# Kernel optimization log

Measured on AMD Instinct MI355X. Metric: run time of the kernel, lower is better.

## Reference

```python
import math
import jax, jax.numpy as jnp
import numpy as np

D_MODEL = 1024
N_HEADS = 16
HEAD_DIM = D_MODEL // N_HEADS
ROPE_BASE = 10000.0
EPS = 1e-6


def rmsnorm(x, w, eps=EPS):
    # x: (..., head_dim); computed in fp32 like the torch code
    xf = x.astype(jnp.float32)
    rms = jax.lax.rsqrt(jnp.mean(xf * xf, axis=-1, keepdims=True) + eps)
    return (xf * rms).astype(x.dtype) * w


def apply_rope(x, cos, sin):
    # x: (B, H, T, head_dim); cos/sin: (T, head_dim/2)
    d2 = x.shape[-1] // 2
    x1, x2 = x[..., :d2], x[..., d2:]
    c = cos[None, None, :, :]
    s = sin[None, None, :, :]
    return jnp.concatenate([x1 * c - x2 * s, x2 * c + x1 * s], axis=-1)


def setup_inputs() -> dict:
    key = jax.random.key(0)
    ks = jax.random.split(key, 7)
    B, T = 2, 2048
    x = jax.random.normal(ks[0], (B, T, D_MODEL), dtype=jnp.float32)
    scale = 1.0 / math.sqrt(D_MODEL)
    Wq = jax.random.normal(ks[1], (D_MODEL, D_MODEL), dtype=jnp.float32) * scale
    Wk = jax.random.normal(ks[2], (D_MODEL, D_MODEL), dtype=jnp.float32) * scale
    Wv = jax.random.normal(ks[3], (D_MODEL, D_MODEL), dtype=jnp.float32) * scale
    Wo = jax.random.normal(ks[4], (D_MODEL, D_MODEL), dtype=jnp.float32) * scale
    q_norm_w = jnp.ones((HEAD_DIM,), dtype=jnp.float32)
    k_norm_w = jnp.ones((HEAD_DIM,), dtype=jnp.float32)
    return {"x": x, "Wq": Wq, "Wk": Wk, "Wv": Wv, "Wo": Wo,
            "q_norm_w": q_norm_w, "k_norm_w": k_norm_w}


def reference(x, Wq, Wk, Wv, Wo, q_norm_w, k_norm_w):
    B, T, d = x.shape
    H, hd = N_HEADS, HEAD_DIM
    # projections (nn.Linear applies x @ W.T; here W is stored as (in,out))
    q = (x @ Wq).reshape(B, T, H, hd).transpose(0, 2, 1, 3)  # (B,H,T,hd)
    k = (x @ Wk).reshape(B, T, H, hd).transpose(0, 2, 1, 3)
    v = (x @ Wv).reshape(B, T, H, hd).transpose(0, 2, 1, 3)
    # QK RMSNorm per head
    q = rmsnorm(q, q_norm_w)
    k = rmsnorm(k, k_norm_w)
    # rotary embeddings
    inv_freq = 1.0 / (ROPE_BASE ** (jnp.arange(0, hd, 2, dtype=jnp.float32) / hd))
    t = jnp.arange(T, dtype=jnp.float32)
    freqs = jnp.outer(t, inv_freq)  # (T, hd/2)
    cos, sin = jnp.cos(freqs), jnp.sin(freqs)
    q = apply_rope(q, cos, sin)
    k = apply_rope(k, cos, sin)
    # naive full attention with causal mask
    scale = 1.0 / math.sqrt(hd)
    attn = jnp.einsum('bhqd,bhkd->bhqk', q, k) * scale  # (B,H,T,T)
    causal = jnp.triu(jnp.full((T, T), -jnp.inf, dtype=attn.dtype), k=1)
    attn = attn + causal[None, None, :, :]
    attn = jax.nn.softmax(attn, axis=-1)
    out = jnp.einsum('bhqk,bhkd->bhqd', attn, v)
    out = out.transpose(0, 2, 1, 3).reshape(B, T, d)
    return out @ Wo
```

## Files before the change

kernel.cpp:

```cpp
#include <hip/hip_runtime.h>

typedef unsigned short u16;
typedef unsigned int   u32;
typedef __bf16 bf16x8 __attribute__((ext_vector_type(8)));
typedef float  f32x4  __attribute__((ext_vector_type(4)));
typedef u32    u32x4  __attribute__((ext_vector_type(4)));
typedef u16    u16x4  __attribute__((ext_vector_type(4)));

#define D_MODEL 1024
#define T_SEQ   2048
#define NH      16
#define HD      64

__device__ __forceinline__ float b2f(u16 u){ return __uint_as_float(((u32)u)<<16); }
__device__ __forceinline__ u16 f2b(float f){
  u32 x = __float_as_uint(f);
  x += 0x7fffu + ((x>>16)&1u);
  return (u16)(x>>16);
}

__device__ __forceinline__ void gll16(const void* g, void* l){
  __builtin_amdgcn_global_load_lds((const __attribute__((address_space(1))) unsigned int*)g,
                                   (__attribute__((address_space(3))) unsigned int*)l, 16, 0, 0);
}

__global__ __launch_bounds__(256) void f32_to_bf16(const float* __restrict__ src, u16* __restrict__ dst)
{
  const int i = (blockIdx.x*256 + threadIdx.x)<<2;
  f32x4 v = *(const f32x4*)(src + i);
  u16x4 o;
  o[0]=f2b(v[0]); o[1]=f2b(v[1]); o[2]=f2b(v[2]); o[3]=f2b(v[3]);
  *(u16x4*)(dst + i) = o;
}

__global__ void transpose_w(const float* __restrict__ W0, const float* __restrict__ W1,
                            const float* __restrict__ W2, const float* __restrict__ W3,
                            u16* __restrict__ T0, u16* __restrict__ T1,
                            u16* __restrict__ T2, u16* __restrict__ T3)
{
  __shared__ u16 s[32][33];
  const int z = blockIdx.z;
  const float* src = (z==0)?W0:(z==1)?W1:(z==2)?W2:W3;
  u16*         dst = (z==0)?T0:(z==1)?T1:(z==2)?T2:T3;
  const int x = threadIdx.x, y = threadIdx.y;
  const int r0 = blockIdx.y*32, c0 = blockIdx.x*32;
  #pragma unroll
  for (int r=0;r<4;r++) s[y + r*8][x] = f2b(src[(r0 + y + r*8)*D_MODEL + c0 + x]);
  __syncthreads();
  #pragma unroll
  for (int r=0;r<4;r++) dst[(c0 + y + r*8)*D_MODEL + r0 + x] = s[x][y + r*8];
}

__global__ __launch_bounds__(256) void gemm128(
    const u16* __restrict__ A,
    const u16* __restrict__ B0, const u16* __restrict__ B1, const u16* __restrict__ B2,
    float* __restrict__ oF, u16* __restrict__ oQ, u16* __restrict__ oK, u16* __restrict__ oVt)
{
  __shared__ __align__(16) u16 sA[512*8];
  __shared__ __align__(16) u16 sB[512*8];
  const int z = blockIdx.z;
  const u16* Bt = (z==0)?B0:(z==1)?B1:B2;

  const int tid = threadIdx.x;
  const int bm0 = blockIdx.y<<7, bn0 = blockIdx.x<<7;
  const int lane = tid & 63;
  const int w  = tid>>6;
  const int wm = (w>>1)<<6;
  const int wn = (w&1)<<6;
  const int quad = lane>>4, lr = lane&15;

  const int s0 = w*64 + lane, s1 = 256 + w*64 + lane;
  const int rA0 = s0>>2, cA0 = (s0&3)^((rA0>>1)&3);
  const int rA1 = s1>>2, cA1 = (s1&3)^((rA1>>1)&3);
  u16* ldsA0 = sA + (w*64)*8;
  u16* ldsA1 = sA + (256 + w*64)*8;
  u16* ldsB0 = sB + (w*64)*8;
  u16* ldsB1 = sB + (256 + w*64)*8;
  const u16* gA0 = A  + (bm0+rA0)*D_MODEL + cA0*8;
  const u16* gA1 = A  + (bm0+rA1)*D_MODEL + cA1*8;
  const u16* gB0 = Bt + (bn0+rA0)*D_MODEL + cA0*8;
  const u16* gB1 = Bt + (bn0+rA1)*D_MODEL + cA1*8;

  const int cfr = (lr>>1)&3;

  const f32x4 z4 = {0.f,0.f,0.f,0.f};
  f32x4 acc[4][4];
  #pragma unroll
  for (int i=0;i<4;i++)
    #pragma unroll
    for (int j=0;j<4;j++) acc[i][j] = z4;

  for (int kt=0; kt<D_MODEL; kt+=32){
    gll16(gA0 + kt, ldsA0);
    gll16(gA1 + kt, ldsA1);
    gll16(gB0 + kt, ldsB0);
    gll16(gB1 + kt, ldsB1);
    __syncthreads();
    bf16x8 af[4], bfr[4];
    const int cq = (quad ^ cfr)<<3;
    #pragma unroll
    for (int i=0;i<4;i++) af[i]  = *(const bf16x8*)(sA + (wm + (i<<4) + lr)*32 + cq);
    #pragma unroll
    for (int j=0;j<4;j++) bfr[j] = *(const bf16x8*)(sB + (wn + (j<<4) + lr)*32 + cq);
    #pragma unroll
    for (int i=0;i<4;i++)
      #pragma unroll
      for (int j=0;j<4;j++)
        acc[i][j] = __builtin_amdgcn_mfma_f32_16x16x32_bf16(af[i], bfr[j], acc[i][j], 0, 0, 0);
    __syncthreads();
  }

  const int rq = quad<<2;
  if (z==2){
    #pragma unroll
    for (int i=0;i<4;i++){
      int row0 = bm0 + wm + (i<<4) + rq;
      int bb = row0 >> 11, tt = row0 & (T_SEQ-1);
      #pragma unroll
      for (int j=0;j<4;j++){
        int col = bn0 + wn + (j<<4) + lr;
        int hh = col >> 6, dd = col & 63;
        u16x4 st;
        #pragma unroll
        for (int r=0;r<4;r++) st[r] = f2b(acc[i][j][r]);
        *(u16x4*)(oVt + ((bb*NH + hh)*HD + dd)*T_SEQ + tt) = st;
      }
    }
  } else {
    u16* oB = (z==0) ? oQ : oK;
    #pragma unroll
    for (int i=0;i<4;i++){
      #pragma unroll
      for (int r=0;r<4;r++){
        int grow = bm0 + wm + (i<<4) + rq + r;
        #pragma unroll
        for (int j=0;j<4;j++){
          int gcol = bn0 + wn + (j<<4) + lr;
          float v = acc[i][j][r];
          if (z==0 && oF) oF[grow*D_MODEL + gcol] = v;
          else            oB[grow*D_MODEL + gcol] = f2b(v);
        }
      }
    }
  }
}

__global__ __launch_bounds__(256) void rmsrope(u16* __restrict__ Q, u16* __restrict__ K,
                                               const float* __restrict__ qw, const float* __restrict__ kw)
{
  const int gtid = blockIdx.x*256 + threadIdx.x;
  const int wave = gtid >> 6;
  const int lane = gtid & 63;
  const int row  = wave >> 4;
  const int h    = wave & 15;
  const int t    = row & (T_SEQ-1);
  const int addr = row*D_MODEL + h*HD + lane;

  const int fi = lane & 31;
  const float inv_freq = __expf(-(float)fi * 0.28782313662f);
  float sn, cs;
  __sincosf((float)t * inv_freq, &sn, &cs);

  {
    float x = b2f(Q[addr]);
    float ss = x*x;
    #pragma unroll
    for (int off=32; off>=1; off>>=1) ss += __shfl_xor(ss, off, 64);
    float rms = rsqrtf(ss*(1.0f/64.0f) + 1e-6f);
    float xn = x*rms*qw[lane];
    float pr = __shfl_xor(xn, 32, 64);
    float ro = (lane<32) ? (xn*cs - pr*sn) : (xn*cs + pr*sn);
    Q[addr] = f2b(ro * 0.125f);
  }
  {
    float x = b2f(K[addr]);
    float ss = x*x;
    #pragma unroll
    for (int off=32; off>=1; off>>=1) ss += __shfl_xor(ss, off, 64);
    float rms = rsqrtf(ss*(1.0f/64.0f) + 1e-6f);
    float xn = x*rms*kw[lane];
    float pr = __shfl_xor(xn, 32, 64);
    K[addr] = f2b((lane<32) ? (xn*cs - pr*sn) : (xn*cs + pr*sn));
  }
}

__global__ __launch_bounds__(256) void attn_mfma(const u16* __restrict__ Qb, const u16* __restrict__ Kb,
                                                 const u16* __restrict__ Vt, u16* __restrict__ AO)
{
  __shared__ __align__(16) u16 sK [2][512*8];
  __shared__ __align__(16) u16 sVT[2][512*8];
  __shared__ __align__(16) u16 sP [4][16*68];
  const int tid = threadIdx.x;
  const int h  = blockIdx.x, b = blockIdx.y;
  const int qt = 31 - blockIdx.z;
  const int w = tid>>6, lane = tid&63;
  const int quad = lane>>4, lr = lane&15;
  const int q8 = quad<<3;

  const int s0 = w*64 + lane, s1 = 256 + w*64 + lane;
  const int r0s = s0>>3, c0s = (s0&7)^(r0s&7);
  const int r1s = s1>>3, c1s = (s1&7)^(r1s&7);
  const u16* Kbase = Kb + (b*T_SEQ)*D_MODEL + h*HD;
  const u16* Vbase = Vt + (b*NH + h)*HD*T_SEQ;
  const int ldsOff0 = (w*64)*8, ldsOff1 = (256 + w*64)*8;

  const u16* Qrow = Qb + (b*T_SEQ + qt*64 + w*16 + lr)*D_MODEL + h*HD;
  bf16x8 qf0 = *(const bf16x8*)(Qrow + q8);
  bf16x8 qf1 = *(const bf16x8*)(Qrow + 32 + q8);

  f32x4 o[4];
  float lp[4];
  const f32x4 z4 = {0.f,0.f,0.f,0.f};
  const f32x4 i8 = {-8.f,-8.f,-8.f,-8.f};
  #pragma unroll
  for (int r=0;r<4;r++) lp[r] = 0.f;
  #pragma unroll
  for (int nt=0;nt<4;nt++) o[nt] = z4;

  u16* myP = sP[w];

  {
    gll16(Kbase + (0*64 + r0s)*D_MODEL + c0s*8, &sK[0][ldsOff0]);
    gll16(Kbase + (0*64 + r1s)*D_MODEL + c1s*8, &sK[0][ldsOff1]);
    gll16(Vbase + r0s*T_SEQ + 0*64 + c0s*8,     &sVT[0][ldsOff0]);
    gll16(Vbase + r1s*T_SEQ + 0*64 + c1s*8,     &sVT[0][ldsOff1]);
  }
  __syncthreads();

  for (int kt=0; kt<=qt; ++kt){
    const int cur = kt&1;
    if (kt < qt){
      const int kn = kt+1, nb = cur^1;
      gll16(Kbase + (kn*64 + r0s)*D_MODEL + c0s*8, &sK[nb][ldsOff0]);
      gll16(Kbase + (kn*64 + r1s)*D_MODEL + c1s*8, &sK[nb][ldsOff1]);
      gll16(Vbase + r0s*T_SEQ + kn*64 + c0s*8,     &sVT[nb][ldsOff0]);
      gll16(Vbase + r1s*T_SEQ + kn*64 + c1s*8,     &sVT[nb][ldsOff1]);
    }

    f32x4 s4[4];
    #pragma unroll
    for (int ct=0; ct<4; ++ct){
      const int row = ct*16 + lr;
      const int sw = row&7;
      bf16x8 k0 = *(const bf16x8*)(&sK[cur][(row*8 + (quad     ^ sw))*8]);
      bf16x8 k1 = *(const bf16x8*)(&sK[cur][(row*8 + ((4+quad) ^ sw))*8]);
      f32x4 acc = i8;
      acc = __builtin_amdgcn_mfma_f32_16x16x32_bf16(qf0, k0, acc, 0,0,0);
      acc = __builtin_amdgcn_mfma_f32_16x16x32_bf16(qf1, k1, acc, 0,0,0);
      s4[ct] = acc;
    }

    if (kt == qt){
      #pragma unroll
      for (int ct=0; ct<4; ++ct){
        int col = ct*16 + lr;
        #pragma unroll
        for (int r=0;r<4;r++)
          if (col > w*16 + quad*4 + r) s4[ct][r] = -1e30f;
      }
    }

    #pragma unroll
    for (int ct=0; ct<4; ++ct){
      #pragma unroll
      for (int r=0;r<4;r++){
        float p = __expf(s4[ct][r]);
        u32 pu = __float_as_uint(p) & 0xffff0000u;
        lp[r] += __uint_as_float(pu);
        myP[(quad*4 + r)*68 + ct*16 + lr] = (u16)(pu>>16);
      }
    }

    #pragma unroll
    for (int st=0; st<2; ++st){
      bf16x8 pf = *(const bf16x8*)(myP + lr*68 + st*32 + q8);
      #pragma unroll
      for (int nt=0;nt<4;nt++){
        const int row = nt*16 + lr;
        const int slot = row*8 + ((st*4+quad) ^ (row&7));
        bf16x8 vf = *(const bf16x8*)(&sVT[cur][slot*8]);
        o[nt] = __builtin_amdgcn_mfma_f32_16x16x32_bf16(pf, vf, o[nt], 0,0,0);
      }
    }
    __syncthreads();
  }

  #pragma unroll
  for (int r=0;r<4;r++){
    #pragma unroll
    for (int off=8; off>=1; off>>=1) lp[r] += __shfl_xor(lp[r], off, 64);
  }
  const int rowg = b*T_SEQ + qt*64 + w*16 + quad*4;
  #pragma unroll
  for (int r=0;r<4;r++){
    float inv = 1.0f / lp[r];
    #pragma unroll
    for (int nt=0;nt<4;nt++)
      AO[(rowg + r)*D_MODEL + h*HD + nt*16 + lr] = f2b(o[nt][r]*inv);
  }
}

extern "C" void kernel_launch(void* const* d_in, const int* in_sizes, int n_in,
                              void* d_out, int out_size, void* d_ws, size_t ws_size,
                              hipStream_t stream)
{
  const float* X  = (const float*)d_in[0];
  const float* Wq = (const float*)d_in[1];
  const float* Wk = (const float*)d_in[2];
  const float* Wv = (const float*)d_in[3];
  const float* Wo = (const float*)d_in[4];
  const float* qw = (const float*)d_in[5];
  const float* kw = (const float*)d_in[6];

  char* ws = (char*)d_ws;
  const size_t MB = 1024*1024;
  u16* WqT = (u16*)(ws + 0*MB);
  u16* WkT = (u16*)(ws + 2*MB);
  u16* WvT = (u16*)(ws + 4*MB);
  u16* WoT = (u16*)(ws + 6*MB);
  u16* Xb  = (u16*)(ws + 8*MB);
  u16* Qb  = (u16*)(ws + 16*MB);
  u16* Kb  = (u16*)(ws + 24*MB);
  u16* Vt  = (u16*)(ws + 32*MB);
  u16* AO  = (u16*)(ws + 40*MB);

  f32_to_bf16<<<dim3(4096), 256, 0, stream>>>(X, Xb);
  transpose_w<<<dim3(32,32,4), dim3(32,8), 0, stream>>>(Wq,Wk,Wv,Wo, WqT,WkT,WvT,WoT);
  gemm128<<<dim3(8,32,3), 256, 0, stream>>>(Xb, WqT, WkT, WvT, nullptr, Qb, Kb, Vt);
  rmsrope<<<dim3(16384), 256, 0, stream>>>(Qb, Kb, qw, kw);
  attn_mfma<<<dim3(NH, 2, 32), 256, 0, stream>>>(Qb, Kb, Vt, AO);
  gemm128<<<dim3(8,32,1), 256, 0, stream>>>(AO, WoT, WoT, WoT, (float*)d_out, nullptr, nullptr, nullptr);
}
```

Measured before the change: 230.2 us.

## Fuse RMSNorm and RoPE into QKV GEMM epilogue with XCD-aware tiling

Removes the separate rmsrope pass by applying per-head RMSNorm and rotary embedding inside the QKV GEMM epilogue, using a precomputed cos/sin table written by a small new kernel. The QKV weights are packed contiguously so a single GEMM covers all three projections. Both GEMMs now use a 64-wide K step with 8-way LDS swizzle and a block-id remap that groups tiles by XCD for better L2 locality. This saves one read-modify-write pass over Q and K and halves the number of barriers, at the cost of more LDS per block and a heavier epilogue.

```diff
diff --git a/kernel.cpp b/kernel.cpp
--- a/kernel.cpp
+++ b/kernel.cpp
@@ -4,6 +4,7 @@
 typedef unsigned int   u32;
 typedef __bf16 bf16x8 __attribute__((ext_vector_type(8)));
 typedef float  f32x4  __attribute__((ext_vector_type(4)));
+typedef float  f32x2  __attribute__((ext_vector_type(2)));
 typedef u32    u32x4  __attribute__((ext_vector_type(4)));
 typedef u16    u16x4  __attribute__((ext_vector_type(4)));
 
@@ -51,37 +52,46 @@
   for (int r=0;r<4;r++) dst[(c0 + y + r*8)*D_MODEL + r0 + x] = s[x][y + r*8];
 }
 
-__global__ __launch_bounds__(256) void gemm128(
-    const u16* __restrict__ A,
-    const u16* __restrict__ B0, const u16* __restrict__ B1, const u16* __restrict__ B2,
-    float* __restrict__ oF, u16* __restrict__ oQ, u16* __restrict__ oK, u16* __restrict__ oVt)
-{
-  __shared__ __align__(16) u16 sA[512*8];
-  __shared__ __align__(16) u16 sB[512*8];
-  const int z = blockIdx.z;
-  const u16* Bt = (z==0)?B0:(z==1)?B1:B2;
+__global__ __launch_bounds__(256) void rope_table(float* __restrict__ cs)
+{
+  const int gid = blockIdx.x*256 + threadIdx.x;
+  const int t = gid >> 5, fi = gid & 31;
+  const float invf = expf(-(float)fi * 0.2878231366242558f);
+  float sn, cn;
+  sincosf((float)t * invf, &sn, &cn);
+  cs[gid*2]   = cn;
+  cs[gid*2+1] = sn;
+}
+
+__global__ __launch_bounds__(256) void gemm_qkv(
+    const u16* __restrict__ A, const u16* __restrict__ Bt,
+    const float* __restrict__ qw, const float* __restrict__ kw,
+    const float* __restrict__ cs,
+    u16* __restrict__ Qb, u16* __restrict__ Kb, u16* __restrict__ Vt)
+{
+  __shared__ __align__(16) u16 sA[1024*8];
+  __shared__ __align__(16) u16 sB[1024*8];
+  const int id = blockIdx.x;
+  const int xcd = id & 7, slot = id >> 3;
+  const int bn = (xcd & 1)*12 + (slot % 12);
+  const int bm = (xcd >> 1)*8 + (slot / 12);
+  const int bm0 = bm<<7, bn0 = bn<<7;
 
   const int tid = threadIdx.x;
-  const int bm0 = blockIdx.y<<7, bn0 = blockIdx.x<<7;
   const int lane = tid & 63;
   const int w  = tid>>6;
   const int wm = (w>>1)<<6;
   const int wn = (w&1)<<6;
   const int quad = lane>>4, lr = lane&15;
-
-  const int s0 = w*64 + lane, s1 = 256 + w*64 + lane;
-  const int rA0 = s0>>2, cA0 = (s0&3)^((rA0>>1)&3);
-  const int rA1 = s1>>2, cA1 = (s1&3)^((rA1>>1)&3);
-  u16* ldsA0 = sA + (w*64)*8;
-  u16* ldsA1 = sA + (256 + w*64)*8;
-  u16* ldsB0 = sB + (w*64)*8;
-  u16* ldsB1 = sB + (256 + w*64)*8;
-  const u16* gA0 = A  + (bm0+rA0)*D_MODEL + cA0*8;
-  const u16* gA1 = A  + (bm0+rA1)*D_MODEL + cA1*8;
-  const u16* gB0 = Bt + (bn0+rA0)*D_MODEL + cA0*8;
-  const u16* gB1 = Bt + (bn0+rA1)*D_MODEL + cA1*8;
-
-  const int cfr = (lr>>1)&3;
+  const int swl = lr & 7;
+
+  int rS[4], cS[4];
+  #pragma unroll
+  for (int i=0;i<4;i++){
+    int s = i*256 + tid;
+    rS[i] = s>>3;
+    cS[i] = (s&7) ^ (rS[i]&7);
+  }
 
   const f32x4 z4 = {0.f,0.f,0.f,0.f};
   f32x4 acc[4][4];
@@ -90,97 +100,157 @@
     #pragma unroll
     for (int j=0;j<4;j++) acc[i][j] = z4;
 
-  for (int kt=0; kt<D_MODEL; kt+=32){
-    gll16(gA0 + kt, ldsA0);
-    gll16(gA1 + kt, ldsA1);
-    gll16(gB0 + kt, ldsB0);
-    gll16(gB1 + kt, ldsB1);
+  for (int kt=0; kt<D_MODEL; kt+=64){
+    #pragma unroll
+    for (int i=0;i<4;i++)
+      gll16(A  + (bm0+rS[i])*D_MODEL + kt + cS[i]*8, sA + (i*256 + w*64)*8);
+    #pragma unroll
+    for (int i=0;i<4;i++)
+      gll16(Bt + (bn0+rS[i])*D_MODEL + kt + cS[i]*8, sB + (i*256 + w*64)*8);
     __syncthreads();
-    bf16x8 af[4], bfr[4];
-    const int cq = (quad ^ cfr)<<3;
-    #pragma unroll
-    for (int i=0;i<4;i++) af[i]  = *(const bf16x8*)(sA + (wm + (i<<4) + lr)*32 + cq);
-    #pragma unroll
-    for (int j=0;j<4;j++) bfr[j] = *(const bf16x8*)(sB + (wn + (j<<4) + lr)*32 + cq);
-    #pragma unroll
-    for (int i=0;i<4;i++)
-      #pragma unroll
-      for (int j=0;j<4;j++)
-        acc[i][j] = __builtin_amdgcn_mfma_f32_16x16x32_bf16(af[i], bfr[j], acc[i][j], 0, 0, 0);
+    #pragma unroll
+    for (int kk=0; kk<2; ++kk){
+      bf16x8 af[4], bfr[4];
+      const int cq = (kk*4 + quad) ^ swl;
+      #pragma unroll
+      for (int i=0;i<4;i++) af[i]  = *(const bf16x8*)(sA + ((wm + (i<<4) + lr)*8 + cq)*8);
+      #pragma unroll
+      for (int j=0;j<4;j++) bfr[j] = *(const bf16x8*)(sB + ((wn + (j<<4) + lr)*8 + cq)*8);
+      #pragma unroll
+      for (int i=0;i<4;i++)
+        #pragma unroll
+        for (int j=0;j<4;j++)
+          acc[i][j] = __builtin_amdgcn_mfma_f32_16x16x32_bf16(af[i], bfr[j], acc[i][j], 0, 0, 0);
+    }
     __syncthreads();
   }
 
+  const int z = bn0 >> 10;
+  const int ncl = bn0 & 1023;
   const int rq = quad<<2;
-  if (z==2){
+
+  if (z == 2){
     #pragma unroll
     for (int i=0;i<4;i++){
       int row0 = bm0 + wm + (i<<4) + rq;
       int bb = row0 >> 11, tt = row0 & (T_SEQ-1);
       #pragma unroll
       for (int j=0;j<4;j++){
-        int col = bn0 + wn + (j<<4) + lr;
-        int hh = col >> 6, dd = col & 63;
+        int nv = ncl + wn + (j<<4) + lr;
+        int hh = nv >> 6, dd = nv & 63;
         u16x4 st;
         #pragma unroll
         for (int r=0;r<4;r++) st[r] = f2b(acc[i][j][r]);
-        *(u16x4*)(oVt + ((bb*NH + hh)*HD + dd)*T_SEQ + tt) = st;
+        *(u16x4*)(Vt + ((bb*NH + hh)*HD + dd)*T_SEQ + tt) = st;
       }
     }
   } else {
-    u16* oB = (z==0) ? oQ : oK;
+    const float* w_ = (z==0) ? qw : kw;
+    u16* dst = (z==0) ? Qb : Kb;
+    const float scale = (z==0) ? 0.125f : 1.0f;
+    float wv[4];
+    #pragma unroll
+    for (int j=0;j<4;j++) wv[j] = w_[(j<<4) + lr];
     #pragma unroll
     for (int i=0;i<4;i++){
       #pragma unroll
       for (int r=0;r<4;r++){
-        int grow = bm0 + wm + (i<<4) + rq + r;
-        #pragma unroll
-        for (int j=0;j<4;j++){
-          int gcol = bn0 + wn + (j<<4) + lr;
-          float v = acc[i][j][r];
-          if (z==0 && oF) oF[grow*D_MODEL + gcol] = v;
-          else            oB[grow*D_MODEL + gcol] = f2b(v);
-        }
+        const int grow = bm0 + wm + (i<<4) + rq + r;
+        float ss = 0.f;
+        #pragma unroll
+        for (int j=0;j<4;j++) ss += acc[i][j][r]*acc[i][j][r];
+        #pragma unroll
+        for (int off=8; off>=1; off>>=1) ss += __shfl_xor(ss, off, 64);
+        const float rms = rsqrtf(ss*(1.0f/64.0f) + 1e-6f);
+        float xn[4];
+        #pragma unroll
+        for (int j=0;j<4;j++) xn[j] = acc[i][j][r]*rms*wv[j];
+        const int t = grow & (T_SEQ-1);
+        f32x2 c0 = *(const f32x2*)(cs + (t*32 + lr)*2);
+        f32x2 c1 = *(const f32x2*)(cs + (t*32 + 16 + lr)*2);
+        float o0 = xn[0]*c0[0] - xn[2]*c0[1];
+        float o2 = xn[2]*c0[0] + xn[0]*c0[1];
+        float o1 = xn[1]*c1[0] - xn[3]*c1[1];
+        float o3 = xn[3]*c1[0] + xn[1]*c1[1];
+        u16* rp = dst + grow*D_MODEL + ncl + wn + lr;
+        rp[0]  = f2b(o0*scale);
+        rp[16] = f2b(o1*scale);
+        rp[32] = f2b(o2*scale);
+        rp[48] = f2b(o3*scale);
       }
     }
   }
 }
 
-__global__ __launch_bounds__(256) void rmsrope(u16* __restrict__ Q, u16* __restrict__ K,
-                                               const float* __restrict__ qw, const float* __restrict__ kw)
-{
-  const int gtid = blockIdx.x*256 + threadIdx.x;
-  const int wave = gtid >> 6;
-  const int lane = gtid & 63;
-  const int row  = wave >> 4;
-  const int h    = wave & 15;
-  const int t    = row & (T_SEQ-1);
-  const int addr = row*D_MODEL + h*HD + lane;
-
-  const int fi = lane & 31;
-  const float inv_freq = __expf(-(float)fi * 0.28782313662f);
-  float sn, cs;
-  __sincosf((float)t * inv_freq, &sn, &cs);
-
-  {
-    float x = b2f(Q[addr]);
-    float ss = x*x;
-    #pragma unroll
-    for (int off=32; off>=1; off>>=1) ss += __shfl_xor(ss, off, 64);
-    float rms = rsqrtf(ss*(1.0f/64.0f) + 1e-6f);
-    float xn = x*rms*qw[lane];
-    float pr = __shfl_xor(xn, 32, 64);
-    float ro = (lane<32) ? (xn*cs - pr*sn) : (xn*cs + pr*sn);
-    Q[addr] = f2b(ro * 0.125f);
-  }
-  {
-    float x = b2f(K[addr]);
-    float ss = x*x;
-    #pragma unroll
-    for (int off=32; off>=1; off>>=1) ss += __shfl_xor(ss, off, 64);
-    float rms = rsqrtf(ss*(1.0f/64.0f) + 1e-6f);
-    float xn = x*rms*kw[lane];
-    float pr = __shfl_xor(xn, 32, 64);
-    K[addr] = f2b((lane<32) ? (xn*cs - pr*sn) : (xn*cs + pr*sn));
+__global__ __launch_bounds__(256) void gemm_out(
+    const u16* __restrict__ A, const u16* __restrict__ Bt, float* __restrict__ out)
+{
+  __shared__ __align__(16) u16 sA[1024*8];
+  __shared__ __align__(16) u16 sB[1024*8];
+  const int id = blockIdx.x;
+  const int xcd = id & 7, slot = id >> 3;
+  const int bn = slot & 7;
+  const int bm = xcd*4 + (slot>>3);
+  const int bm0 = bm<<7, bn0 = bn<<7;
+
+  const int tid = threadIdx.x;
+  const int lane = tid & 63;
+  const int w  = tid>>6;
+  const int wm = (w>>1)<<6;
+  const int wn = (w&1)<<6;
+  const int quad = lane>>4, lr = lane&15;
+  const int swl = lr & 7;
+
+  int rS[4], cS[4];
+  #pragma unroll
+  for (int i=0;i<4;i++){
+    int s = i*256 + tid;
+    rS[i] = s>>3;
+    cS[i] = (s&7) ^ (rS[i]&7);
+  }
+
+  const f32x4 z4 = {0.f,0.f,0.f,0.f};
+  f32x4 acc[4][4];
+  #pragma unroll
+  for (int i=0;i<4;i++)
+    #pragma unroll
+    for (int j=0;j<4;j++) acc[i][j] = z4;
+
+  for (int kt=0; kt<D_MODEL; kt+=64){
+    #pragma unroll
+    for (int i=0;i<4;i++)
+      gll16(A  + (bm0+rS[i])*D_MODEL + kt + cS[i]*8, sA + (i*256 + w*64)*8);
+    #pragma unroll
+    for (int i=0;i<4;i++)
+      gll16(Bt + (bn0+rS[i])*D_MODEL + kt + cS[i]*8, sB + (i*256 + w*64)*8);
+    __syncthreads();
+    #pragma unroll
+    for (int kk=0; kk<2; ++kk){
+      bf16x8 af[4], bfr[4];
+      const int cq = (kk*4 + quad) ^ swl;
+      #pragma unroll
+      for (int i=0;i<4;i++) af[i]  = *(const bf16x8*)(sA + ((wm + (i<<4) + lr)*8 + cq)*8);
+      #pragma unroll
+      for (int j=0;j<4;j++) bfr[j] = *(const bf16x8*)(sB + ((wn + (j<<4) + lr)*8 + cq)*8);
+      #pragma unroll
+      for (int i=0;i<4;i++)
+        #pragma unroll
+        for (int j=0;j<4;j++)
+          acc[i][j] = __builtin_amdgcn_mfma_f32_16x16x32_bf16(af[i], bfr[j], acc[i][j], 0, 0, 0);
+    }
+    __syncthreads();
+  }
+
+  const int rq = quad<<2;
+  #pragma unroll
+  for (int i=0;i<4;i++){
+    #pragma unroll
+    for (int r=0;r<4;r++){
+      const int grow = bm0 + wm + (i<<4) + rq + r;
+      #pragma unroll
+      for (int j=0;j<4;j++)
+        out[grow*D_MODEL + bn0 + wn + (j<<4) + lr] = acc[i][j][r];
+    }
   }
 }
 
@@ -219,12 +289,10 @@
 
   u16* myP = sP[w];
 
-  {
-    gll16(Kbase + (0*64 + r0s)*D_MODEL + c0s*8, &sK[0][ldsOff0]);
-    gll16(Kbase + (0*64 + r1s)*D_MODEL + c1s*8, &sK[0][ldsOff1]);
-    gll16(Vbase + r0s*T_SEQ + 0*64 + c0s*8,     &sVT[0][ldsOff0]);
-    gll16(Vbase + r1s*T_SEQ + 0*64 + c1s*8,     &sVT[0][ldsOff1]);
-  }
+  gll16(Kbase + r0s*D_MODEL + c0s*8, &sK[0][ldsOff0]);
+  gll16(Kbase + r1s*D_MODEL + c1s*8, &sK[0][ldsOff1]);
+  gll16(Vbase + r0s*T_SEQ + c0s*8,   &sVT[0][ldsOff0]);
+  gll16(Vbase + r1s*T_SEQ + c1s*8,   &sVT[0][ldsOff1]);
   __syncthreads();
 
   for (int kt=0; kt<=qt; ++kt){
@@ -314,20 +382,20 @@
 
   char* ws = (char*)d_ws;
   const size_t MB = 1024*1024;
-  u16* WqT = (u16*)(ws + 0*MB);
-  u16* WkT = (u16*)(ws + 2*MB);
-  u16* WvT = (u16*)(ws + 4*MB);
-  u16* WoT = (u16*)(ws + 6*MB);
-  u16* Xb  = (u16*)(ws + 8*MB);
-  u16* Qb  = (u16*)(ws + 16*MB);
-  u16* Kb  = (u16*)(ws + 24*MB);
-  u16* Vt  = (u16*)(ws + 32*MB);
-  u16* AO  = (u16*)(ws + 40*MB);
+  u16*   WqkvT = (u16*)(ws + 0*MB);
+  u16*   WoT   = (u16*)(ws + 6*MB);
+  u16*   Xb    = (u16*)(ws + 8*MB);
+  u16*   Qb    = (u16*)(ws + 16*MB);
+  u16*   Kb    = (u16*)(ws + 24*MB);
+  u16*   Vt    = (u16*)(ws + 32*MB);
+  u16*   AO    = (u16*)(ws + 40*MB);
+  float* CS    = (float*)(ws + 48*MB);
 
   f32_to_bf16<<<dim3(4096), 256, 0, stream>>>(X, Xb);
-  transpose_w<<<dim3(32,32,4), dim3(32,8), 0, stream>>>(Wq,Wk,Wv,Wo, WqT,WkT,WvT,WoT);
-  gemm128<<<dim3(8,32,3), 256, 0, stream>>>(Xb, WqT, WkT, WvT, nullptr, Qb, Kb, Vt);
-  rmsrope<<<dim3(16384), 256, 0, stream>>>(Qb, Kb, qw, kw);
+  transpose_w<<<dim3(32,32,4), dim3(32,8), 0, stream>>>(
+      Wq,Wk,Wv,Wo, WqkvT, WqkvT + 1024*1024, WqkvT + 2*1024*1024, WoT);
+  rope_table<<<dim3(256), 256, 0, stream>>>(CS);
+  gemm_qkv<<<dim3(768), 256, 0, stream>>>(Xb, WqkvT, qw, kw, CS, Qb, Kb, Vt);
   attn_mfma<<<dim3(NH, 2, 32), 256, 0, stream>>>(Qb, Kb, Vt, AO);
-  gemm128<<<dim3(8,32,1), 256, 0, stream>>>(AO, WoT, WoT, WoT, (float*)d_out, nullptr, nullptr, nullptr);
-}
+  gemm_out<<<dim3(256), 256, 0, stream>>>(AO, WoT, (float*)d_out);
+}
```

After: 204.4 us. 11.2% less time.
